# Kernel tuning notes

Hardware: AMD Instinct MI355X
Metric: run time of the kernel (lower is better)

The kernel has to match this reference:

```python
import jax, jax.numpy as jnp
import numpy as np

K = 3
PAD = 1


def bilinear_gather(xr, py, px):
    # xr: [B, G, H, W, C] channels-last per offset group; py/px: [B, G, H, W] sample coords
    B, G, H, W, C = xr.shape
    y0 = jnp.floor(py)
    x0 = jnp.floor(px)
    wy = py - y0
    wx = px - x0
    y0i = y0.astype(jnp.int32)
    x0i = x0.astype(jnp.int32)
    bi = jnp.arange(B)[:, None, None, None]
    gi = jnp.arange(G)[None, :, None, None]
    out = jnp.zeros(py.shape + (C,), xr.dtype)
    corners = (
        (0, 0, (1 - wy) * (1 - wx)),
        (0, 1, (1 - wy) * wx),
        (1, 0, wy * (1 - wx)),
        (1, 1, wy * wx),
    )
    for dy_, dx_, w in corners:
        yy = y0i + dy_
        xx = x0i + dx_
        valid = ((yy >= 0) & (yy < H) & (xx >= 0) & (xx < W)).astype(xr.dtype)
        yc = jnp.clip(yy, 0, H - 1)
        xc = jnp.clip(xx, 0, W - 1)
        v = xr[bi, gi, yc, xc]  # [B,G,H,W,C]
        out = out + (w * valid)[..., None] * v
    return out


def setup_inputs() -> dict:
    key = jax.random.key(0)
    k1, k2, k3, k4, k5 = jax.random.split(key, 5)
    B, Cin, H, W = 4, 64, 256, 256
    G, OC = 8, 64
    KK = K * K
    x = jax.random.normal(k1, (B, Cin, H, W), jnp.float32)
    offset = jax.random.normal(k2, (B, 2, G * KK, H, W), jnp.float32)
    mask = jax.random.normal(k3, (B, G * KK, H, W), jnp.float32)
    weight = jax.random.normal(k4, (OC, Cin // G, K, K), jnp.float32) * 0.05
    bias = jax.random.normal(k5, (OC,), jnp.float32) * 0.01
    return {"x": x, "offset": offset, "mask": mask, "weight": weight, "bias": bias}


def reference(x, offset, mask, weight, bias):
    B, Cin, H, W = x.shape
    OC, Cpg, _, _ = weight.shape
    G = Cin // Cpg          # conv groups == offset groups here
    OPG = OC // G
    KK = K * K
    # replicate module's permute(0,2,1,3,4).flip(1).view(b,-1,fh,fw):
    # pair axis (dy,dx) is input dim 1; combined (group,tap) axis is reversed
    off = jnp.flip(offset, axis=2)                      # [B,2,G*KK,H,W]
    dy = off[:, 0].reshape(B, G, KK, H, W)
    dx = off[:, 1].reshape(B, G, KK, H, W)
    m = jax.nn.sigmoid(mask).reshape(B, G, KK, H, W)
    xr = x.reshape(B, G, Cpg, H, W).transpose(0, 1, 3, 4, 2)  # [B,G,H,W,Cpg]
    wg = weight.reshape(G, OPG, Cpg, K, K)
    iy = jnp.arange(H, dtype=x.dtype)[None, None, :, None]
    ix = jnp.arange(W, dtype=x.dtype)[None, None, None, :]
    out = jnp.zeros((B, G, OPG, H, W), x.dtype)
    for t in range(KK):  # fixed small loop over kernel taps
        ki, kj = t // K, t % K
        py = iy - PAD + ki + dy[:, :, t]
        px = ix - PAD + kj + dx[:, :, t]
        s = bilinear_gather(xr, py, px) * m[:, :, t][..., None]  # [B,G,H,W,Cpg]
        out = out + jnp.einsum('bghwc,gdc->bgdhw', s, wg[:, :, :, ki, kj])
    return out.reshape(B, OC, H, W) + bias[None, :, None, None]
```

## Files before the change

### kernel.cpp

```cpp
#include <hip/hip_runtime.h>
#include <hip/hip_fp16.h>


#define KSZ 3
#define PAD 1

static constexpr int B   = 4;
static constexpr int Cin = 64;
static constexpr int H   = 256;
static constexpr int W   = 256;
static constexpr int G   = 8;
static constexpr int OC  = 64;
static constexpr int KK  = KSZ * KSZ;
static constexpr int Cpg = Cin / G;
static constexpr int OPG = OC / G;
static constexpr int HW  = H * W;
static constexpr int NXCD = 8;

static constexpr int BR    = 4;
static constexpr int BC    = 64;
static constexpr int MARG  = 5;
static constexpr int WROWS = BR + 2 * MARG + 1;
static constexpr int WCOLS = 75;
static constexpr int WUSED = BC + 2 * MARG;

typedef _Float16 f16x8  __attribute__((ext_vector_type(8)));
typedef float    f32x16 __attribute__((ext_vector_type(16)));

union U4H {
    uint4 u;
    __half2 h2[4];
    _Float16 h[8];
    f16x8 v;
};

struct Pend {
    float wy, wx, ms;
    int   iy0, ix0;
    bool  ok;
    uint4 c00, c01, c10, c11;
};

__global__ __launch_bounds__(256) void transpose_kernel(
    const float* __restrict__ x, uint4* __restrict__ xt)
{
    const int h = blockIdx.x, g = blockIdx.y, b = blockIdx.z;
    const int w = threadIdx.x;
    const int pix = h * W + w;
    const float* src = x + (size_t)(b * Cin + g * Cpg) * HW + pix;
    U4H v;
#pragma unroll
    for (int c = 0; c < 8; ++c) v.h[c] = (_Float16)src[(size_t)c * HW];
    xt[(size_t)(b * G + g) * HW + pix] = v.u;
}

__global__ __launch_bounds__(320) void prep_weights(
    const float* __restrict__ weight, uint4* __restrict__ wfrag)
{
    const int g    = blockIdx.x;
    const int tid  = threadIdx.x;
    const int m    = tid >> 6;
    const int lane = tid & 63;
    const int hi   = lane >> 5;
    const int lp   = lane & 31;
    const int t    = 2 * m + hi;
    U4H a;
#pragma unroll
    for (int c = 0; c < 8; ++c) {
        float v = 0.0f;
        if (lp < OPG && t < KK)
            v = weight[((size_t)(g * OPG + lp) * Cpg + c) * KK + t];
        a.h[c] = (_Float16)v;
    }
    wfrag[((size_t)g * 5 + m) * 64 + lane] = a.u;
}

__global__ __launch_bounds__(256) void dcn_kernel(
    const uint4* __restrict__ xt,
    const uint4* __restrict__ wfrag,
    const float* __restrict__ offset,
    const float* __restrict__ mask,
    const float* __restrict__ bias,
    float* __restrict__ out)
{
    __shared__ uint4 win[WROWS * WCOLS];

    const unsigned id = blockIdx.x;
    const unsigned wl = (id & (NXCD - 1)) * (gridDim.x / NXCD) + (id >> 3);
    const int colblk = wl & 3;
    const int rowblk = (wl >> 2) & 63;
    const int g      = (wl >> 8) & (G - 1);
    const int b      = wl >> 11;

    const int h_base = rowblk * BR;
    const int xbase  = colblk * BC;
    const int h0     = h_base - MARG;
    const int x0base = xbase - MARG;

    const int tid  = threadIdx.x;
    const int lane = tid & 63;
    const int wave = tid >> 6;
    const int hi   = lane >> 5;
    const int lp   = lane & 31;

    const int h = h_base + wave;

    const uint4* xb = xt + (size_t)(b * G + g) * HW;

#pragma unroll
    for (int it = 0; it < 5; ++it) {
        const int k = it * 256 + tid;
        if (k < WROWS * WCOLS) {
            const int i = k / WCOLS;
            const int j = k - i * WCOLS;
            const int gr = h0 + i;
            const int gc = x0base + j;
            const bool vld = ((unsigned)gr < (unsigned)H) & ((unsigned)gc < (unsigned)W);
            const int grc = min(max(gr, 0), H - 1);
            const int gcc = min(max(gc, 0), W - 1);
            uint4 val = xb[grc * W + gcc];
            if (!vld) val = make_uint4(0, 0, 0, 0);
            win[k] = val;
        }
    }

    f16x8 afrag[5];
    {
        const uint4* wf = wfrag + (size_t)g * 5 * 64 + lane;
#pragma unroll
        for (int m = 0; m < 5; ++m) {
            U4H tmp; tmp.u = wf[m * 64];
            afrag[m] = tmp.v;
        }
    }

    const float* offy = offset + (size_t)(b * 2 + 0) * (G * KK) * HW;
    const float* offx = offset + (size_t)(b * 2 + 1) * (G * KK) * HW;
    const float* mk   = mask + (size_t)b * (G * KK) * HW;

    float dyv[2][5], dxv[2][5], msv[2][5];
#pragma unroll
    for (int tile = 0; tile < 2; ++tile) {
        const int wq  = xbase + tile * 32 + lp;
        const int pix = h * W + wq;
#pragma unroll
        for (int m = 0; m < 5; ++m) {
            const int t  = 2 * m + hi;
            const int tt = (t > 8) ? 8 : t;
            const int idx0 = G * KK - 1 - (g * KK + tt);
            dyv[tile][m] = offy[(size_t)idx0 * HW + pix];
            dxv[tile][m] = offx[(size_t)idx0 * HW + pix];
            const float mv = mk[(size_t)(g * KK + tt) * HW + pix];
            float s = 1.0f / (1.0f + __expf(-mv));
            msv[tile][m] = (t <= 8) ? s : 0.0f;
        }
    }

    float pyb[5], pxb0[5], pxb1[5];
#pragma unroll
    for (int m = 0; m < 5; ++m) {
        const int t  = 2 * m + hi;
        const int tt = (t > 8) ? 8 : t;
        const int ki = (tt >= 3) + (tt >= 6);
        const int kj = tt - 3 * ki;
        pyb[m]  = (float)(h - PAD + ki);
        pxb0[m] = (float)(xbase + lp - PAD + kj);
        pxb1[m] = pxb0[m] + 32.0f;
    }

    __syncthreads();

    auto issue = [&](float pybm, float pxbm, float dy, float dx, float ms) -> Pend {
        Pend p;
        const float py = pybm + dy;
        const float px = pxbm + dx;
        const float y0f = floorf(py), x0f = floorf(px);
        p.wy = py - y0f;
        p.wx = px - x0f;
        p.ms = ms;
        p.iy0 = (int)y0f - h0;
        p.ix0 = (int)x0f - x0base;
        p.ok = ((unsigned)p.iy0 <= (unsigned)(WROWS - 2)) &
               ((unsigned)p.ix0 <= (unsigned)(WUSED - 2));
        int a0 = p.iy0 * WCOLS + p.ix0;
        a0 = p.ok ? a0 : 0;
        p.c00 = win[a0];         p.c01 = win[a0 + 1];
        p.c10 = win[a0 + WCOLS]; p.c11 = win[a0 + WCOLS + 1];
        return p;
    };

    auto finish = [&](Pend p) -> f16x8 {
        const float u  = (1.f - p.wy) * p.ms;
        const float vv = p.wy * p.ms;
        const float cx0 = 1.f - p.wx, cx1 = p.wx;
        float w00 = u * cx0, w01 = u * cx1, w10 = vv * cx0, w11 = vv * cx1;
        if (__builtin_expect(!__all((int)p.ok), 0)) {
            if (!p.ok) {
                const int y0 = p.iy0 + h0, x0 = p.ix0 + x0base;
                const bool vy0 = (y0 >= 0) & (y0 < H), vy1 = (y0 + 1 >= 0) & (y0 + 1 < H);
                const bool vx0 = (x0 >= 0) & (x0 < W), vx1 = (x0 + 1 >= 0) & (x0 + 1 < W);
                const float uu = vy0 ? u : 0.f,  vz = vy1 ? vv : 0.f;
                const float ca = vx0 ? cx0 : 0.f, cb = vx1 ? cx1 : 0.f;
                w00 = uu * ca; w01 = uu * cb; w10 = vz * ca; w11 = vz * cb;
                const int yc0 = min(max(y0, 0), H - 1), yc1 = min(max(y0 + 1, 0), H - 1);
                const int xc0 = min(max(x0, 0), W - 1), xc1 = min(max(x0 + 1, 0), W - 1);
                p.c00 = xb[yc0 * W + xc0]; p.c01 = xb[yc0 * W + xc1];
                p.c10 = xb[yc1 * W + xc0]; p.c11 = xb[yc1 * W + xc1];
            }
        }
        U4H a, bq, c, d; a.u = p.c00; bq.u = p.c01; c.u = p.c10; d.u = p.c11;
        const __half2 h00 = __float2half2_rn(w00);
        const __half2 h01 = __float2half2_rn(w01);
        const __half2 h10 = __float2half2_rn(w10);
        const __half2 h11 = __float2half2_rn(w11);
        U4H s;
#pragma unroll
        for (int i = 0; i < 4; ++i)
            s.h2[i] = __hfma2(h00, a.h2[i],
                      __hfma2(h01, bq.h2[i],
                      __hfma2(h10, c.h2[i],
                      __hmul2(h11, d.h2[i]))));
        return s.v;
    };

    f32x16 acc0 = {};
    f32x16 acc1 = {};
#pragma unroll
    for (int m = 0; m < 5; ++m) {
        Pend p0 = issue(pyb[m], pxb0[m], dyv[0][m], dxv[0][m], msv[0][m]);
        Pend p1 = issue(pyb[m], pxb1[m], dyv[1][m], dxv[1][m], msv[1][m]);
        acc0 = __builtin_amdgcn_mfma_f32_32x32x16_f16(afrag[m], finish(p0), acc0, 0, 0, 0);
        acc1 = __builtin_amdgcn_mfma_f32_32x32x16_f16(afrag[m], finish(p1), acc1, 0, 0, 0);
    }

#pragma unroll
    for (int tile = 0; tile < 2; ++tile) {
        const int wq = xbase + tile * 32 + lp;
#pragma unroll
        for (int r = 0; r < 4; ++r) {
            const int dd = r + 4 * hi;
            const float v = (tile == 0 ? acc0[r] : acc1[r]) + bias[g * OPG + dd];
            out[((size_t)b * OC + g * OPG + dd) * HW + h * W + wq] = v;
        }
    }
}

extern "C" void kernel_launch(void* const* d_in, const int* in_sizes, int n_in,
                              void* d_out, int out_size, void* d_ws, size_t ws_size,
                              hipStream_t stream) {
    const float* x      = (const float*)d_in[0];
    const float* offset = (const float*)d_in[1];
    const float* mask   = (const float*)d_in[2];
    const float* weight = (const float*)d_in[3];
    const float* bias   = (const float*)d_in[4];
    float* out = (float*)d_out;

    uint4* xt    = (uint4*)d_ws;
    uint4* wfrag = (uint4*)((char*)d_ws + (size_t)B * G * HW * 16);

    dim3 tgrid(H, G, B);
    transpose_kernel<<<tgrid, dim3(256), 0, stream>>>(x, xt);
    prep_weights<<<dim3(G), dim3(320), 0, stream>>>(weight, wfrag);
    dcn_kernel<<<dim3(B * G * (H / BR) * (W / BC)), dim3(256), 0, stream>>>(
        xt, wfrag, offset, mask, bias, out);
}
```

Baseline: 106.2 us.

## Process four row-tiles per block with a rolling 16-row LDS ring window

```diff
diff --git a/kernel.cpp b/kernel.cpp
--- a/kernel.cpp
+++ b/kernel.cpp
@@ -18,11 +18,11 @@
 static constexpr int NXCD = 8;
 
 static constexpr int BR    = 4;
+static constexpr int TPB   = 4;
 static constexpr int BC    = 64;
-static constexpr int MARG  = 5;
-static constexpr int WROWS = BR + 2 * MARG + 1;
+static constexpr int WRING = 16;
 static constexpr int WCOLS = 75;
-static constexpr int WUSED = BC + 2 * MARG;
+static constexpr int WUSED = 74;
 
 typedef _Float16 f16x8  __attribute__((ext_vector_type(8)));
 typedef float    f32x16 __attribute__((ext_vector_type(16)));
@@ -32,13 +32,6 @@
     __half2 h2[4];
     _Float16 h[8];
     f16x8 v;
-};
-
-struct Pend {
-    float wy, wx, ms;
-    int   iy0, ix0;
-    bool  ok;
-    uint4 c00, c01, c10, c11;
 };
 
 __global__ __launch_bounds__(256) void transpose_kernel(
@@ -83,19 +76,18 @@
     const float* __restrict__ bias,
     float* __restrict__ out)
 {
-    __shared__ uint4 win[WROWS * WCOLS];
+    __shared__ uint4 win[WRING * WCOLS];
 
     const unsigned id = blockIdx.x;
     const unsigned wl = (id & (NXCD - 1)) * (gridDim.x / NXCD) + (id >> 3);
-    const int colblk = wl & 3;
-    const int rowblk = (wl >> 2) & 63;
-    const int g      = (wl >> 8) & (G - 1);
-    const int b      = wl >> 11;
-
-    const int h_base = rowblk * BR;
-    const int xbase  = colblk * BC;
-    const int h0     = h_base - MARG;
-    const int x0base = xbase - MARG;
+    const int q      = wl & 15;
+    const int colblk = (wl >> 4) & 3;
+    const int g      = (wl >> 6) & (G - 1);
+    const int b      = wl >> 9;
+
+    const int h_start = q * (BR * TPB);
+    const int xbase   = colblk * BC;
+    const int x0base  = xbase - 5;
 
     const int tid  = threadIdx.x;
     const int lane = tid & 63;
@@ -103,24 +95,22 @@
     const int hi   = lane >> 5;
     const int lp   = lane & 31;
 
-    const int h = h_base + wave;
-
     const uint4* xb = xt + (size_t)(b * G + g) * HW;
 
 #pragma unroll
     for (int it = 0; it < 5; ++it) {
         const int k = it * 256 + tid;
-        if (k < WROWS * WCOLS) {
+        if (k < WRING * WCOLS) {
             const int i = k / WCOLS;
             const int j = k - i * WCOLS;
-            const int gr = h0 + i;
+            const int y  = h_start - 5 + i;
             const int gc = x0base + j;
-            const bool vld = ((unsigned)gr < (unsigned)H) & ((unsigned)gc < (unsigned)W);
-            const int grc = min(max(gr, 0), H - 1);
+            const bool vld = ((unsigned)y < (unsigned)H) & ((unsigned)gc < (unsigned)W);
+            const int yc = min(max(y, 0), H - 1);
             const int gcc = min(max(gc, 0), W - 1);
-            uint4 val = xb[grc * W + gcc];
+            uint4 val = xb[yc * W + gcc];
             if (!vld) val = make_uint4(0, 0, 0, 0);
-            win[k] = val;
+            win[(y & 15) * WCOLS + j] = val;
         }
     }
 
@@ -138,77 +128,42 @@
     const float* offx = offset + (size_t)(b * 2 + 1) * (G * KK) * HW;
     const float* mk   = mask + (size_t)b * (G * KK) * HW;
 
-    float dyv[2][5], dxv[2][5], msv[2][5];
-#pragma unroll
-    for (int tile = 0; tile < 2; ++tile) {
-        const int wq  = xbase + tile * 32 + lp;
-        const int pix = h * W + wq;
-#pragma unroll
-        for (int m = 0; m < 5; ++m) {
-            const int t  = 2 * m + hi;
-            const int tt = (t > 8) ? 8 : t;
-            const int idx0 = G * KK - 1 - (g * KK + tt);
-            dyv[tile][m] = offy[(size_t)idx0 * HW + pix];
-            dxv[tile][m] = offx[(size_t)idx0 * HW + pix];
-            const float mv = mk[(size_t)(g * KK + tt) * HW + pix];
-            float s = 1.0f / (1.0f + __expf(-mv));
-            msv[tile][m] = (t <= 8) ? s : 0.0f;
-        }
-    }
-
-    float pyb[5], pxb0[5], pxb1[5];
-#pragma unroll
-    for (int m = 0; m < 5; ++m) {
-        const int t  = 2 * m + hi;
-        const int tt = (t > 8) ? 8 : t;
-        const int ki = (tt >= 3) + (tt >= 6);
-        const int kj = tt - 3 * ki;
-        pyb[m]  = (float)(h - PAD + ki);
-        pxb0[m] = (float)(xbase + lp - PAD + kj);
-        pxb1[m] = pxb0[m] + 32.0f;
-    }
-
-    __syncthreads();
-
-    auto issue = [&](float pybm, float pxbm, float dy, float dx, float ms) -> Pend {
-        Pend p;
-        const float py = pybm + dy;
-        const float px = pxbm + dx;
+    auto sample = [&](int hb5, float py, float px, float ms) -> f16x8 {
         const float y0f = floorf(py), x0f = floorf(px);
-        p.wy = py - y0f;
-        p.wx = px - x0f;
-        p.ms = ms;
-        p.iy0 = (int)y0f - h0;
-        p.ix0 = (int)x0f - x0base;
-        p.ok = ((unsigned)p.iy0 <= (unsigned)(WROWS - 2)) &
-               ((unsigned)p.ix0 <= (unsigned)(WUSED - 2));
-        int a0 = p.iy0 * WCOLS + p.ix0;
-        a0 = p.ok ? a0 : 0;
-        p.c00 = win[a0];         p.c01 = win[a0 + 1];
-        p.c10 = win[a0 + WCOLS]; p.c11 = win[a0 + WCOLS + 1];
-        return p;
-    };
-
-    auto finish = [&](Pend p) -> f16x8 {
-        const float u  = (1.f - p.wy) * p.ms;
-        const float vv = p.wy * p.ms;
-        const float cx0 = 1.f - p.wx, cx1 = p.wx;
-        float w00 = u * cx0, w01 = u * cx1, w10 = vv * cx0, w11 = vv * cx1;
-        if (__builtin_expect(!__all((int)p.ok), 0)) {
-            if (!p.ok) {
-                const int y0 = p.iy0 + h0, x0 = p.ix0 + x0base;
-                const bool vy0 = (y0 >= 0) & (y0 < H), vy1 = (y0 + 1 >= 0) & (y0 + 1 < H);
-                const bool vx0 = (x0 >= 0) & (x0 < W), vx1 = (x0 + 1 >= 0) & (x0 + 1 < W);
+        const float wy = py - y0f, wx = px - x0f;
+        const int y0  = (int)y0f, x0 = (int)x0f;
+        const int ix0 = x0 - x0base;
+        const bool ok = ((unsigned)(y0 - hb5) <= 14u) & ((unsigned)ix0 <= 72u);
+        int a0 = (y0 & 15) * WCOLS + ix0;
+        int a1 = ((y0 + 1) & 15) * WCOLS + ix0;
+        a0 = ok ? a0 : 0;
+        a1 = ok ? a1 : 0;
+        uint4 c00 = win[a0], c01 = win[a0 + 1];
+        uint4 c10 = win[a1], c11 = win[a1 + 1];
+
+        const float u  = (1.f - wy) * ms;
+        const float vv = wy * ms;
+        float w00 = u * (1.f - wx), w01 = u * wx;
+        float w10 = vv * (1.f - wx), w11 = vv * wx;
+
+        if (__builtin_expect(!__all((int)ok), 0)) {
+            if (!ok) {
+                const bool vy0 = (unsigned)y0 < (unsigned)H;
+                const bool vy1 = (unsigned)(y0 + 1) < (unsigned)H;
+                const bool vx0 = (unsigned)x0 < (unsigned)W;
+                const bool vx1 = (unsigned)(x0 + 1) < (unsigned)W;
                 const float uu = vy0 ? u : 0.f,  vz = vy1 ? vv : 0.f;
-                const float ca = vx0 ? cx0 : 0.f, cb = vx1 ? cx1 : 0.f;
+                const float ca = vx0 ? (1.f - wx) : 0.f;
+                const float cb = vx1 ? wx : 0.f;
                 w00 = uu * ca; w01 = uu * cb; w10 = vz * ca; w11 = vz * cb;
                 const int yc0 = min(max(y0, 0), H - 1), yc1 = min(max(y0 + 1, 0), H - 1);
                 const int xc0 = min(max(x0, 0), W - 1), xc1 = min(max(x0 + 1, 0), W - 1);
-                p.c00 = xb[yc0 * W + xc0]; p.c01 = xb[yc0 * W + xc1];
-                p.c10 = xb[yc1 * W + xc0]; p.c11 = xb[yc1 * W + xc1];
-            }
-        }
-        U4H a, bq, c, d; a.u = p.c00; bq.u = p.c01; c.u = p.c10; d.u = p.c11;
+                c00 = xb[yc0 * W + xc0]; c01 = xb[yc0 * W + xc1];
+                c10 = xb[yc1 * W + xc0]; c11 = xb[yc1 * W + xc1];
+            }
+        }
+
+        U4H a, bq, c, d; a.u = c00; bq.u = c01; c.u = c10; d.u = c11;
         const __half2 h00 = __float2half2_rn(w00);
         const __half2 h01 = __float2half2_rn(w01);
         const __half2 h10 = __float2half2_rn(w10);
@@ -223,25 +178,87 @@
         return s.v;
     };
 
-    f32x16 acc0 = {};
-    f32x16 acc1 = {};
-#pragma unroll
-    for (int m = 0; m < 5; ++m) {
-        Pend p0 = issue(pyb[m], pxb0[m], dyv[0][m], dxv[0][m], msv[0][m]);
-        Pend p1 = issue(pyb[m], pxb1[m], dyv[1][m], dxv[1][m], msv[1][m]);
-        acc0 = __builtin_amdgcn_mfma_f32_32x32x16_f16(afrag[m], finish(p0), acc0, 0, 0, 0);
-        acc1 = __builtin_amdgcn_mfma_f32_32x32x16_f16(afrag[m], finish(p1), acc1, 0, 0, 0);
-    }
-
-#pragma unroll
-    for (int tile = 0; tile < 2; ++tile) {
-        const int wq = xbase + tile * 32 + lp;
-#pragma unroll
-        for (int r = 0; r < 4; ++r) {
-            const int dd = r + 4 * hi;
-            const float v = (tile == 0 ? acc0[r] : acc1[r]) + bias[g * OPG + dd];
-            out[((size_t)b * OC + g * OPG + dd) * HW + h * W + wq] = v;
-        }
+    __syncthreads();
+
+    const int pi0 = tid / WCOLS, pj0 = tid - pi0 * WCOLS;
+    const int k1  = 256 + tid;
+    const int pi1 = k1 / WCOLS, pj1 = k1 - pi1 * WCOLS;
+    const bool has1 = (k1 < BR * WCOLS + 256) & (k1 < 300 + 256) & (tid < 44);
+
+#pragma unroll 1
+    for (int s = 0; s < TPB; ++s) {
+        const int h_base = h_start + BR * s;
+        const int h   = h_base + wave;
+        const int hb5 = h_base - 5;
+
+        float dyv[2][5], dxv[2][5], msv[2][5];
+#pragma unroll
+        for (int tile = 0; tile < 2; ++tile) {
+            const int wq  = xbase + tile * 32 + lp;
+            const int pix = h * W + wq;
+#pragma unroll
+            for (int m = 0; m < 5; ++m) {
+                const int t  = 2 * m + hi;
+                const int tt = (t > 8) ? 8 : t;
+                const int idx0 = G * KK - 1 - (g * KK + tt);
+                dyv[tile][m] = offy[(size_t)idx0 * HW + pix];
+                dxv[tile][m] = offx[(size_t)idx0 * HW + pix];
+                const float mv = mk[(size_t)(g * KK + tt) * HW + pix];
+                float sg = 1.0f / (1.0f + __expf(-mv));
+                msv[tile][m] = (t <= 8) ? sg : 0.0f;
+            }
+        }
+
+        uint4 pf0 = make_uint4(0, 0, 0, 0), pf1 = make_uint4(0, 0, 0, 0);
+        int yA = 0, yB = 0;
+        bool pv0 = false, pv1 = false;
+        if (s < TPB - 1) {
+            yA = h_base + 11 + pi0;
+            const int gcA = x0base + pj0;
+            pv0 = ((unsigned)yA < (unsigned)H) & ((unsigned)gcA < (unsigned)W);
+            pf0 = xb[min(max(yA, 0), H - 1) * W + min(max(gcA, 0), W - 1)];
+            if (has1) {
+                yB = h_base + 11 + pi1;
+                const int gcB = x0base + pj1;
+                pv1 = ((unsigned)yB < (unsigned)H) & ((unsigned)gcB < (unsigned)W);
+                pf1 = xb[min(max(yB, 0), H - 1) * W + min(max(gcB, 0), W - 1)];
+            }
+        }
+
+        f32x16 acc0 = {};
+        f32x16 acc1 = {};
+#pragma unroll
+        for (int m = 0; m < 5; ++m) {
+            const int t  = 2 * m + hi;
+            const int tt = (t > 8) ? 8 : t;
+            const int ki = (tt >= 3) + (tt >= 6);
+            const int kj = tt - 3 * ki;
+            const float pyb = (float)(h - PAD + ki);
+            const float pxb = (float)(xbase + lp - PAD + kj);
+            acc0 = __builtin_amdgcn_mfma_f32_32x32x16_f16(
+                afrag[m], sample(hb5, pyb + dyv[0][m], pxb + dxv[0][m], msv[0][m]), acc0, 0, 0, 0);
+            acc1 = __builtin_amdgcn_mfma_f32_32x32x16_f16(
+                afrag[m], sample(hb5, pyb + dyv[1][m], pxb + 32.0f + dxv[1][m], msv[1][m]), acc1, 0, 0, 0);
+        }
+
+#pragma unroll
+        for (int tile = 0; tile < 2; ++tile) {
+            const int wq = xbase + tile * 32 + lp;
+#pragma unroll
+            for (int r = 0; r < 4; ++r) {
+                const int dd = r + 4 * hi;
+                const float v = (tile == 0 ? acc0[r] : acc1[r]) + bias[g * OPG + dd];
+                out[((size_t)b * OC + g * OPG + dd) * HW + h * W + wq] = v;
+            }
+        }
+
+        __syncthreads();
+        if (s < TPB - 1) {
+            win[(yA & 15) * WCOLS + pj0] = pv0 ? pf0 : make_uint4(0, 0, 0, 0);
+            if (has1)
+                win[(yB & 15) * WCOLS + pj1] = pv1 ? pf1 : make_uint4(0, 0, 0, 0);
+        }
+        __syncthreads();
     }
 }
 
@@ -261,6 +278,6 @@
     dim3 tgrid(H, G, B);
     transpose_kernel<<<tgrid, dim3(256), 0, stream>>>(x, xt);
     prep_weights<<<dim3(G), dim3(320), 0, stream>>>(weight, wfrag);
-    dcn_kernel<<<dim3(B * G * (H / BR) * (W / BC)), dim3(256), 0, stream>>>(
+    dcn_kernel<<<dim3(B * G * (H / (BR * TPB)) * (W / BC)), dim3(256), 0, stream>>>(
         xt, wfrag, offset, mask, bias, out);
 }
```

Measured after the change: 96.62 us. 1.1x faster.

## Prefetch per-tap offsets one iteration ahead in a rolled loop to cut registers

Applied to the files above, without the earlier changes.

```diff
diff --git a/kernel.cpp b/kernel.cpp
--- a/kernel.cpp
+++ b/kernel.cpp
@@ -34,13 +34,6 @@
     f16x8 v;
 };
 
-struct Pend {
-    float wy, wx, ms;
-    int   iy0, ix0;
-    bool  ok;
-    uint4 c00, c01, c10, c11;
-};
-
 __global__ __launch_bounds__(256) void transpose_kernel(
     const float* __restrict__ x, uint4* __restrict__ xt)
 {
@@ -73,6 +66,39 @@
         a.h[c] = (_Float16)v;
     }
     wfrag[((size_t)g * 5 + m) * 64 + lane] = a.u;
+}
+
+__device__ __attribute__((noinline)) f16x8 slow_sample(
+    const uint4* __restrict__ xb, int y0, int x0, float wy, float wx, float ms)
+{
+    const bool vy0 = (unsigned)y0 < (unsigned)H;
+    const bool vy1 = (unsigned)(y0 + 1) < (unsigned)H;
+    const bool vx0 = (unsigned)x0 < (unsigned)W;
+    const bool vx1 = (unsigned)(x0 + 1) < (unsigned)W;
+    const float u  = vy0 ? (1.f - wy) * ms : 0.f;
+    const float vv = vy1 ? wy * ms : 0.f;
+    const float ca = vx0 ? (1.f - wx) : 0.f;
+    const float cb = vx1 ? wx : 0.f;
+    const float w00 = u * ca, w01 = u * cb, w10 = vv * ca, w11 = vv * cb;
+    const int yc0 = min(max(y0, 0), H - 1), yc1 = min(max(y0 + 1, 0), H - 1);
+    const int xc0 = min(max(x0, 0), W - 1), xc1 = min(max(x0 + 1, 0), W - 1);
+    U4H a, bq, c, d;
+    a.u  = xb[yc0 * W + xc0];
+    bq.u = xb[yc0 * W + xc1];
+    c.u  = xb[yc1 * W + xc0];
+    d.u  = xb[yc1 * W + xc1];
+    const __half2 h00 = __float2half2_rn(w00);
+    const __half2 h01 = __float2half2_rn(w01);
+    const __half2 h10 = __float2half2_rn(w10);
+    const __half2 h11 = __float2half2_rn(w11);
+    U4H s;
+#pragma unroll
+    for (int i = 0; i < 4; ++i)
+        s.h2[i] = __hfma2(h00, a.h2[i],
+                  __hfma2(h01, bq.h2[i],
+                  __hfma2(h10, c.h2[i],
+                  __hmul2(h11, d.h2[i]))));
+    return s.v;
 }
 
 __global__ __launch_bounds__(256) void dcn_kernel(
@@ -124,91 +150,44 @@
         }
     }
 
-    f16x8 afrag[5];
-    {
-        const uint4* wf = wfrag + (size_t)g * 5 * 64 + lane;
-#pragma unroll
-        for (int m = 0; m < 5; ++m) {
-            U4H tmp; tmp.u = wf[m * 64];
-            afrag[m] = tmp.v;
-        }
-    }
-
     const float* offy = offset + (size_t)(b * 2 + 0) * (G * KK) * HW;
     const float* offx = offset + (size_t)(b * 2 + 1) * (G * KK) * HW;
     const float* mk   = mask + (size_t)b * (G * KK) * HW;
-
-    float dyv[2][5], dxv[2][5], msv[2][5];
-#pragma unroll
-    for (int tile = 0; tile < 2; ++tile) {
-        const int wq  = xbase + tile * 32 + lp;
-        const int pix = h * W + wq;
-#pragma unroll
-        for (int m = 0; m < 5; ++m) {
-            const int t  = 2 * m + hi;
-            const int tt = (t > 8) ? 8 : t;
-            const int idx0 = G * KK - 1 - (g * KK + tt);
-            dyv[tile][m] = offy[(size_t)idx0 * HW + pix];
-            dxv[tile][m] = offx[(size_t)idx0 * HW + pix];
-            const float mv = mk[(size_t)(g * KK + tt) * HW + pix];
-            float s = 1.0f / (1.0f + __expf(-mv));
-            msv[tile][m] = (t <= 8) ? s : 0.0f;
-        }
-    }
-
-    float pyb[5], pxb0[5], pxb1[5];
-#pragma unroll
-    for (int m = 0; m < 5; ++m) {
-        const int t  = 2 * m + hi;
-        const int tt = (t > 8) ? 8 : t;
-        const int ki = (tt >= 3) + (tt >= 6);
-        const int kj = tt - 3 * ki;
-        pyb[m]  = (float)(h - PAD + ki);
-        pxb0[m] = (float)(xbase + lp - PAD + kj);
-        pxb1[m] = pxb0[m] + 32.0f;
+    const uint4* wfb  = wfrag + (size_t)g * 5 * 64 + lane;
+
+    const int pix0 = h * W + xbase + lp;
+    const int pix1 = pix0 + 32;
+
+    float dy0c, dx0c, mv0c, dy1c, dx1c, mv1c;
+    U4H afc;
+    {
+        const int t0  = hi;
+        const int oI = (G * KK - 1 - (g * KK + t0)) * HW;
+        const int mI = (g * KK + t0) * HW;
+        dy0c = offy[oI + pix0];  dx0c = offx[oI + pix0];  mv0c = mk[mI + pix0];
+        dy1c = offy[oI + pix1];  dx1c = offx[oI + pix1];  mv1c = mk[mI + pix1];
+        afc.u = wfb[0];
     }
 
     __syncthreads();
 
-    auto issue = [&](float pybm, float pxbm, float dy, float dx, float ms) -> Pend {
-        Pend p;
-        const float py = pybm + dy;
-        const float px = pxbm + dx;
+    auto sample = [&](float py, float px, float ms) -> f16x8 {
         const float y0f = floorf(py), x0f = floorf(px);
-        p.wy = py - y0f;
-        p.wx = px - x0f;
-        p.ms = ms;
-        p.iy0 = (int)y0f - h0;
-        p.ix0 = (int)x0f - x0base;
-        p.ok = ((unsigned)p.iy0 <= (unsigned)(WROWS - 2)) &
-               ((unsigned)p.ix0 <= (unsigned)(WUSED - 2));
-        int a0 = p.iy0 * WCOLS + p.ix0;
-        a0 = p.ok ? a0 : 0;
-        p.c00 = win[a0];         p.c01 = win[a0 + 1];
-        p.c10 = win[a0 + WCOLS]; p.c11 = win[a0 + WCOLS + 1];
-        return p;
-    };
-
-    auto finish = [&](Pend p) -> f16x8 {
-        const float u  = (1.f - p.wy) * p.ms;
-        const float vv = p.wy * p.ms;
-        const float cx0 = 1.f - p.wx, cx1 = p.wx;
-        float w00 = u * cx0, w01 = u * cx1, w10 = vv * cx0, w11 = vv * cx1;
-        if (__builtin_expect(!__all((int)p.ok), 0)) {
-            if (!p.ok) {
-                const int y0 = p.iy0 + h0, x0 = p.ix0 + x0base;
-                const bool vy0 = (y0 >= 0) & (y0 < H), vy1 = (y0 + 1 >= 0) & (y0 + 1 < H);
-                const bool vx0 = (x0 >= 0) & (x0 < W), vx1 = (x0 + 1 >= 0) & (x0 + 1 < W);
-                const float uu = vy0 ? u : 0.f,  vz = vy1 ? vv : 0.f;
-                const float ca = vx0 ? cx0 : 0.f, cb = vx1 ? cx1 : 0.f;
-                w00 = uu * ca; w01 = uu * cb; w10 = vz * ca; w11 = vz * cb;
-                const int yc0 = min(max(y0, 0), H - 1), yc1 = min(max(y0 + 1, 0), H - 1);
-                const int xc0 = min(max(x0, 0), W - 1), xc1 = min(max(x0 + 1, 0), W - 1);
-                p.c00 = xb[yc0 * W + xc0]; p.c01 = xb[yc0 * W + xc1];
-                p.c10 = xb[yc1 * W + xc0]; p.c11 = xb[yc1 * W + xc1];
-            }
-        }
-        U4H a, bq, c, d; a.u = p.c00; bq.u = p.c01; c.u = p.c10; d.u = p.c11;
+        const float wy = py - y0f, wx = px - x0f;
+        const int y0 = (int)y0f, x0 = (int)x0f;
+        const int iy0 = y0 - h0;
+        const int ix0 = x0 - x0base;
+        const bool ok = ((unsigned)iy0 <= (unsigned)(WROWS - 2)) &
+                        ((unsigned)ix0 <= (unsigned)(WUSED - 2));
+        int a0 = iy0 * WCOLS + ix0;
+        a0 = ok ? a0 : 0;
+        U4H a, bq, c, d;
+        a.u  = win[a0];          bq.u = win[a0 + 1];
+        c.u  = win[a0 + WCOLS];  d.u  = win[a0 + WCOLS + 1];
+        const float u  = (1.f - wy) * ms;
+        const float vv = wy * ms;
+        const float w00 = u * (1.f - wx), w01 = u * wx;
+        const float w10 = vv * (1.f - wx), w11 = vv * wx;
         const __half2 h00 = __float2half2_rn(w00);
         const __half2 h01 = __float2half2_rn(w01);
         const __half2 h10 = __float2half2_rn(w10);
@@ -220,17 +199,51 @@
                       __hfma2(h01, bq.h2[i],
                       __hfma2(h10, c.h2[i],
                       __hmul2(h11, d.h2[i]))));
-        return s.v;
+        f16x8 res = s.v;
+        if (__builtin_expect(!__all((int)ok), 0)) {
+            if (!ok) res = slow_sample(xb, y0, x0, wy, wx, ms);
+        }
+        return res;
     };
 
     f32x16 acc0 = {};
     f32x16 acc1 = {};
-#pragma unroll
+
+#pragma unroll 1
     for (int m = 0; m < 5; ++m) {
-        Pend p0 = issue(pyb[m], pxb0[m], dyv[0][m], dxv[0][m], msv[0][m]);
-        Pend p1 = issue(pyb[m], pxb1[m], dyv[1][m], dxv[1][m], msv[1][m]);
-        acc0 = __builtin_amdgcn_mfma_f32_32x32x16_f16(afrag[m], finish(p0), acc0, 0, 0, 0);
-        acc1 = __builtin_amdgcn_mfma_f32_32x32x16_f16(afrag[m], finish(p1), acc1, 0, 0, 0);
+        const int mn  = (m < 4) ? m + 1 : 4;
+        const int tn  = 2 * mn + hi;
+        const int ttn = (tn > 8) ? 8 : tn;
+        const int oIn = (G * KK - 1 - (g * KK + ttn)) * HW;
+        const int mIn = (g * KK + ttn) * HW;
+        const float dy0n = offy[oIn + pix0];
+        const float dx0n = offx[oIn + pix0];
+        const float mv0n = mk[mIn + pix0];
+        const float dy1n = offy[oIn + pix1];
+        const float dx1n = offx[oIn + pix1];
+        const float mv1n = mk[mIn + pix1];
+        U4H afn; afn.u = wfb[mn * 64];
+
+        const int t  = 2 * m + hi;
+        const int tt = (t > 8) ? 8 : t;
+        const int ki = (tt >= 3) + (tt >= 6);
+        const int kj = tt - 3 * ki;
+        const float pyb = (float)(h - PAD + ki);
+        const float pxb = (float)(xbase + lp - PAD + kj);
+
+        float sg0 = 1.0f / (1.0f + __expf(-mv0c));
+        float sg1 = 1.0f / (1.0f + __expf(-mv1c));
+        sg0 = (t <= 8) ? sg0 : 0.0f;
+        sg1 = (t <= 8) ? sg1 : 0.0f;
+
+        acc0 = __builtin_amdgcn_mfma_f32_32x32x16_f16(
+            afc.v, sample(pyb + dy0c, pxb + dx0c, sg0), acc0, 0, 0, 0);
+        acc1 = __builtin_amdgcn_mfma_f32_32x32x16_f16(
+            afc.v, sample(pyb + dy1c, pxb + 32.0f + dx1c, sg1), acc1, 0, 0, 0);
+
+        dy0c = dy0n; dx0c = dx0n; mv0c = mv0n;
+        dy1c = dy1n; dx1c = dx1n; mv1c = mv1n;
+        afc = afn;
     }
 
 #pragma unroll
```

Result: faster. 99.40 us (-6.5%).
